# Kernel tuning notes

Hardware: AMD Instinct MI355X
Metric: run time of the kernel (lower is better)

Reference implementation:

```python
import jax, jax.numpy as jnp
import numpy as np

D_MODEL = 1024
NUM_HEADS = 16
D_K = D_MODEL // NUM_HEADS


def setup_inputs() -> dict:
    key = jax.random.key(0)
    ks = jax.random.split(key, 11)
    B, T = 4, 2048
    s = 1.0 / np.sqrt(D_MODEL)
    return {
        'query': jax.random.normal(ks[0], (B, T, D_MODEL), jnp.float32),
        'key': jax.random.normal(ks[1], (B, T, D_MODEL), jnp.float32),
        'value': jax.random.normal(ks[2], (B, T, D_MODEL), jnp.float32),
        'Wq': jax.random.normal(ks[3], (D_MODEL, D_MODEL), jnp.float32) * s,
        'bq': jnp.zeros((D_MODEL,), jnp.float32),
        'Wk': jax.random.normal(ks[4], (D_MODEL, D_MODEL), jnp.float32) * s,
        'bk': jnp.zeros((D_MODEL,), jnp.float32),
        'Wv': jax.random.normal(ks[5], (D_MODEL, D_MODEL), jnp.float32) * s,
        'bv': jnp.zeros((D_MODEL,), jnp.float32),
        'Wo': jax.random.normal(ks[6], (D_MODEL, D_MODEL), jnp.float32) * s,
        'bo': jnp.zeros((D_MODEL,), jnp.float32),
    }


def reference(query, key, value, Wq, bq, Wk, bk, Wv, bv, Wo, bo):
    B, Tq, _ = query.shape
    Tk = key.shape[1]
    # projections (torch Linear: x @ W.T + b)
    q = (query @ Wq.T + bq).reshape(B, Tq, NUM_HEADS, D_K).transpose(0, 2, 1, 3)
    k = (key @ Wk.T + bk).reshape(B, Tk, NUM_HEADS, D_K).transpose(0, 2, 1, 3)
    v = (value @ Wv.T + bv).reshape(B, Tk, NUM_HEADS, D_K).transpose(0, 2, 1, 3)
    scale = 1.0 / jnp.sqrt(jnp.asarray(D_K, q.dtype))
    scores = jnp.einsum('bhqd,bhkd->bhqk', q, k) * scale  # [B,H,Tq,Tk]
    attn = jax.nn.softmax(scores, axis=-1)
    out = jnp.einsum('bhqk,bhkd->bhqd', attn, v)
    out = out.transpose(0, 2, 1, 3).reshape(B, Tq, D_MODEL)
    return out @ Wo.T + bo
```

## Files before the change

### kernel.cpp

```cpp
#include <hip/hip_runtime.h>

typedef unsigned short u16;
typedef unsigned int u32;
typedef __attribute__((ext_vector_type(8))) short bf16x8;
typedef __attribute__((ext_vector_type(4))) float f32x4;

__device__ inline u16 f2bf(float x) {
  union { float f; unsigned u; } v; v.f = x;
  unsigned r = v.u + 0x7fffu + ((v.u >> 16) & 1u);
  return (u16)(r >> 16);
}

__device__ inline u32 packbf2(float p0, float p1) {
  return __builtin_amdgcn_perm(__float_as_uint(p1), __float_as_uint(p0), 0x07060302u);
}

__device__ inline void gload16(const void* g, void* l) {
  __builtin_amdgcn_global_load_lds(
      (const __attribute__((address_space(1))) unsigned int*)g,
      (__attribute__((address_space(3))) unsigned int*)l,
      16, 0, 0);
}

__global__ void cvt_bf16_multi(const float* __restrict__ s0, const float* __restrict__ s1,
                               const float* __restrict__ s2, const float* __restrict__ s3,
                               u16* __restrict__ d0, u16* __restrict__ d1,
                               u16* __restrict__ d2, u16* __restrict__ d3, int n4) {
  int i = blockIdx.x * blockDim.x + threadIdx.x;
  if (i >= n4) return;
  int t = blockIdx.y;
  const float* src = (t == 0) ? s0 : (t == 1) ? s1 : (t == 2) ? s2 : s3;
  u16* dst = (t == 0) ? d0 : (t == 1) ? d1 : (t == 2) ? d2 : d3;
  float4 v = ((const float4*)src)[i];
  ushort4 o;
  o.x = f2bf(v.x); o.y = f2bf(v.y); o.z = f2bf(v.z); o.w = f2bf(v.w);
  ((ushort4*)dst)[i] = o;
}

template<int MODE>
__global__ __launch_bounds__(256, 2) void gemm_bt(
    const u16* __restrict__ A, const u16* __restrict__ W,
    const float* __restrict__ bias, void* __restrict__ Cout)
{
  constexpr int N = 1024, K = 1024, BK = 32, NT = K / BK;
  __shared__ __align__(16) u16 As[2][128 * BK];
  __shared__ __align__(16) u16 Bs[2][128 * BK];
  const int tid = threadIdx.x;
  const int wave = tid >> 6, lane = tid & 63;
  const int quad = lane >> 4, l16 = lane & 15;
  const int m0 = blockIdx.x * 128, n0 = blockIdx.y * 128;

  const int sA = wave * 2;
  const int srow = lane >> 2;
  const int skcol = ((lane & 3) ^ (srow & 3)) * 8;
  const int mloc = sA * 16 + srow;
  const int arow = (MODE == 1) ? ((mloc & 64) + (mloc & 3) * 16 + ((mloc & 63) >> 2)) : mloc;
  const int astep = (MODE == 1) ? 4 : 16;
  const u16* ag = A + (size_t)(m0 + arow) * K + skcol;
  const u16* bg = W + (size_t)(n0 + mloc) * K + skcol;

  const int wm = (wave >> 1) * 64, wn = (wave & 1) * 64;
  f32x4 acc[4][4] = {};

  gload16(ag, As[0] + sA * 512);
  gload16(ag + (size_t)astep * K, As[0] + sA * 512 + 512);
  gload16(bg, Bs[0] + sA * 512);
  gload16(bg + 16 * K, Bs[0] + sA * 512 + 512);
  ag += BK; bg += BK;
  __syncthreads();

  int cur = 0;
  for (int kt = 0; kt < NT; ++kt) {
    if (kt + 1 < NT) {
      const int nb = cur ^ 1;
      gload16(ag, As[nb] + sA * 512);
      gload16(ag + (size_t)astep * K, As[nb] + sA * 512 + 512);
      gload16(bg, Bs[nb] + sA * 512);
      gload16(bg + 16 * K, Bs[nb] + sA * 512 + 512);
      ag += BK; bg += BK;
    }
    const u16* Ac = As[cur];
    const u16* Bc = Bs[cur];
    bf16x8 af[4], bf[4];
#pragma unroll
    for (int mi = 0; mi < 4; ++mi)
      af[mi] = *(const bf16x8*)(Ac + (wm + mi * 16 + l16) * BK + ((quad ^ (l16 & 3)) * 8));
#pragma unroll
    for (int ni = 0; ni < 4; ++ni)
      bf[ni] = *(const bf16x8*)(Bc + (wn + ni * 16 + l16) * BK + ((quad ^ (l16 & 3)) * 8));
#pragma unroll
    for (int mi = 0; mi < 4; ++mi)
#pragma unroll
      for (int ni = 0; ni < 4; ++ni)
        acc[mi][ni] = __builtin_amdgcn_mfma_f32_16x16x32_bf16(af[mi], bf[ni], acc[mi][ni], 0, 0, 0);
    __syncthreads();
    cur ^= 1;
  }

#pragma unroll
  for (int ni = 0; ni < 4; ++ni) {
    const int col = n0 + wn + ni * 16 + l16;
    const float bv = bias[col];
#pragma unroll
    for (int mi = 0; mi < 4; ++mi) {
      const int mrow = m0 + wm + mi * 16 + quad * 4;
      f32x4 a = acc[mi][ni];
      if (MODE == 2) {
        float* C = (float*)Cout;
#pragma unroll
        for (int r = 0; r < 4; ++r)
          C[(size_t)(mrow + r) * N + col] = a[r] + bv;
      } else if (MODE == 0) {
        u16* C = (u16*)Cout;
#pragma unroll
        for (int r = 0; r < 4; ++r)
          C[(size_t)(mrow + r) * N + col] = f2bf(a[r] + bv);
      } else {
        u16* C = (u16*)Cout;
        const int bq = mrow >> 11, t = mrow & 2047;
        const int h = col >> 6, d = col & 63;
        ushort4 pk;
        pk.x = f2bf(a[0] + bv); pk.y = f2bf(a[1] + bv);
        pk.z = f2bf(a[2] + bv); pk.w = f2bf(a[3] + bv);
        *(ushort4*)(C + ((size_t)((bq * 16 + h) * 64 + d)) * 2048 + t) = pk;
      }
    }
  }
}

__global__ __launch_bounds__(512, 4) void flash_attn(
    const u16* __restrict__ Qp, const u16* __restrict__ Kp,
    const u16* __restrict__ Vt, u16* __restrict__ Ctx)
{
  constexpr int TQ = 2048, DM = 1024, DK = 64;
  constexpr int KP = 72;
  constexpr int VP = 136;
  constexpr int PP = 68;
  __shared__ __align__(16) u16 Ks[128 * KP];
  __shared__ __align__(16) u16 Vts[64 * VP];
  __shared__ __align__(16) u16 Ps[8][16 * PP];

  const int bh = blockIdx.x, b = bh >> 4, h = bh & 15;
  const int qt = blockIdx.y;
  const int tid = threadIdx.x, wave = tid >> 6, lane = tid & 63;
  const int quad = lane >> 4, l16 = lane & 15;
  const int q0 = qt * 256 + wave * 32;

  bf16x8 qf[2][2];
#pragma unroll
  for (int mi = 0; mi < 2; ++mi)
#pragma unroll
    for (int ks = 0; ks < 2; ++ks)
      qf[mi][ks] = *(const bf16x8*)(Qp + (size_t)(b * TQ + q0 + mi * 16 + l16) * DM
                                       + h * DK + ks * 32 + quad * 8);

  f32x4 O[2][4] = {};
  f32x4 lsum[2] = {};
  const float CS = 0.18033688011112042f;
  const float C0 = 0.0028153f;

  bf16x8 onesv;
#pragma unroll
  for (int j = 0; j < 8; ++j) onesv[j] = (short)0x3F80;

  for (int kt = 0; kt < TQ / 128; ++kt) {
    const int k0 = kt * 128;
#pragma unroll
    for (int i = 0; i < 2; ++i) {
      int c = tid + i * 512;
      int row = c >> 3, seg = c & 7;
      *(float4*)(Ks + row * KP + seg * 8) =
          *(const float4*)(Kp + (size_t)(b * TQ + k0 + row) * DM + h * DK + seg * 8);
    }
#pragma unroll
    for (int i = 0; i < 2; ++i) {
      int c = tid + i * 512;
      int d = c >> 4, seg = c & 15;
      *(float4*)(Vts + d * VP + seg * 8) =
          *(const float4*)(Vt + ((size_t)(bh * DK + d)) * TQ + k0 + seg * 8);
    }
    __syncthreads();

#pragma unroll
    for (int g = 0; g < 2; ++g) {
      f32x4 Sg[2][4];
#pragma unroll
      for (int cc = 0; cc < 4; ++cc) {
        const int c = g * 4 + cc;
        bf16x8 kf0 = *(const bf16x8*)(Ks + (c * 16 + l16) * KP + quad * 8);
        bf16x8 kf1 = *(const bf16x8*)(Ks + (c * 16 + l16) * KP + 32 + quad * 8);
#pragma unroll
        for (int mi = 0; mi < 2; ++mi) {
          f32x4 z = {};
          z = __builtin_amdgcn_mfma_f32_16x16x32_bf16(qf[mi][0], kf0, z, 0, 0, 0);
          Sg[mi][cc] = __builtin_amdgcn_mfma_f32_16x16x32_bf16(qf[mi][1], kf1, z, 0, 0, 0);
        }
      }
      bf16x8 pf[2][2];
#pragma unroll
      for (int mi = 0; mi < 2; ++mi) {
#pragma unroll
        for (int r = 0; r < 4; ++r) {
          float e0 = __builtin_amdgcn_exp2f(fmaf(Sg[mi][0][r], CS, C0));
          float e1 = __builtin_amdgcn_exp2f(fmaf(Sg[mi][1][r], CS, C0));
          float e2 = __builtin_amdgcn_exp2f(fmaf(Sg[mi][2][r], CS, C0));
          float e3 = __builtin_amdgcn_exp2f(fmaf(Sg[mi][3][r], CS, C0));
          uint2 pk;
          pk.x = packbf2(e0, e1);
          pk.y = packbf2(e2, e3);
          *(uint2*)(&Ps[wave][(quad * 4 + r) * PP + l16 * 4]) = pk;
        }
#pragma unroll
        for (int ksl = 0; ksl < 2; ++ksl)
          pf[mi][ksl] = *(const bf16x8*)(&Ps[wave][l16 * PP + ksl * 32 + quad * 8]);
#pragma unroll
        for (int ksl = 0; ksl < 2; ++ksl)
          lsum[mi] = __builtin_amdgcn_mfma_f32_16x16x32_bf16(pf[mi][ksl], onesv, lsum[mi], 0, 0, 0);
      }
#pragma unroll
      for (int ksl = 0; ksl < 2; ++ksl)
#pragma unroll
        for (int ni = 0; ni < 4; ++ni) {
          bf16x8 vf = *(const bf16x8*)(Vts + (ni * 16 + l16) * VP
                                           + g * 64 + ksl * 32 + quad * 8);
          O[0][ni] = __builtin_amdgcn_mfma_f32_16x16x32_bf16(pf[0][ksl], vf, O[0][ni], 0, 0, 0);
          O[1][ni] = __builtin_amdgcn_mfma_f32_16x16x32_bf16(pf[1][ksl], vf, O[1][ni], 0, 0, 0);
        }
    }
    __syncthreads();
  }

#pragma unroll
  for (int mi = 0; mi < 2; ++mi)
#pragma unroll
    for (int r = 0; r < 4; ++r) {
      const float inv = 1.0f / lsum[mi][r];
      const int q = q0 + mi * 16 + quad * 4 + r;
#pragma unroll
      for (int ni = 0; ni < 4; ++ni) {
        const int col = h * DK + ni * 16 + l16;
        Ctx[(size_t)(b * TQ + q) * DM + col] = f2bf(O[mi][ni][r] * inv);
      }
    }
}

extern "C" void kernel_launch(void* const* d_in, const int* in_sizes, int n_in,
                              void* d_out, int out_size, void* d_ws, size_t ws_size,
                              hipStream_t stream)
{
  (void)in_sizes; (void)n_in; (void)out_size; (void)ws_size;
  const float* query = (const float*)d_in[0];
  const float* key_  = (const float*)d_in[1];
  const float* value = (const float*)d_in[2];
  const float* Wq = (const float*)d_in[3];
  const float* bq = (const float*)d_in[4];
  const float* Wk = (const float*)d_in[5];
  const float* bk = (const float*)d_in[6];
  const float* Wv = (const float*)d_in[7];
  const float* bv = (const float*)d_in[8];
  const float* Wo = (const float*)d_in[9];
  const float* bo = (const float*)d_in[10];

  const size_t MT = (size_t)4 * 2048 * 1024;
  const size_t WT = (size_t)1024 * 1024;
  u16* ws  = (u16*)d_ws;
  u16* Xq  = ws;
  u16* Xk  = Xq + MT;
  u16* Xv  = Xk + MT;
  u16* Wqb = Xv + MT;
  u16* Wkb = Wqb + WT;
  u16* Wvb = Wkb + WT;
  u16* Wob = Wvb + WT;
  u16* Qp  = Wob + WT;
  u16* Kp  = Qp + MT;
  u16* Vt  = Kp + MT;
  u16* Ctx = Vt + MT;

  cvt_bf16_multi<<<dim3(8192, 3), 256, 0, stream>>>(
      query, key_, value, value, Xq, Xk, Xv, Xv, (int)(MT / 4));
  cvt_bf16_multi<<<dim3(1024, 4), 256, 0, stream>>>(
      Wq, Wk, Wv, Wo, Wqb, Wkb, Wvb, Wob, (int)(WT / 4));

  dim3 gg(64, 8);
  gemm_bt<0><<<gg, 256, 0, stream>>>(Xq, Wqb, bq, Qp);
  gemm_bt<0><<<gg, 256, 0, stream>>>(Xk, Wkb, bk, Kp);
  gemm_bt<1><<<gg, 256, 0, stream>>>(Xv, Wvb, bv, Vt);

  flash_attn<<<dim3(64, 8), 512, 0, stream>>>(Qp, Kp, Vt, Ctx);

  gemm_bt<2><<<gg, 256, 0, stream>>>(Ctx, Wob, bo, (float*)d_out);
}
```

Baseline: 351.1 us.

## Batch QKV GEMMs, merge conversions, double-buffer flash attention K/V loads

The two conversion kernels are merged into one launch, and the three QKV projection GEMMs become a single launch over a z-dimension grid with occupancy hint 3. The flash attention kernel now double-buffers its K/V tiles using async global-to-LDS loads, with XOR swizzling in place of padding, and raises wave priority around the MFMA sections. The goal is fewer launches, more waves resident at once, and memory latency hidden behind compute. The cost is more shared memory in attention and more complex swizzled indexing.

```diff
diff --git a/kernel.cpp b/kernel.cpp
--- a/kernel.cpp
+++ b/kernel.cpp
@@ -22,19 +22,121 @@
       16, 0, 0);
 }
 
-__global__ void cvt_bf16_multi(const float* __restrict__ s0, const float* __restrict__ s1,
-                               const float* __restrict__ s2, const float* __restrict__ s3,
-                               u16* __restrict__ d0, u16* __restrict__ d1,
-                               u16* __restrict__ d2, u16* __restrict__ d3, int n4) {
-  int i = blockIdx.x * blockDim.x + threadIdx.x;
-  if (i >= n4) return;
-  int t = blockIdx.y;
-  const float* src = (t == 0) ? s0 : (t == 1) ? s1 : (t == 2) ? s2 : s3;
-  u16* dst = (t == 0) ? d0 : (t == 1) ? d1 : (t == 2) ? d2 : d3;
-  float4 v = ((const float4*)src)[i];
+__global__ void cvt_all(const float* __restrict__ q, const float* __restrict__ k,
+                        const float* __restrict__ v,
+                        const float* __restrict__ wq, const float* __restrict__ wk,
+                        const float* __restrict__ wv, const float* __restrict__ wo,
+                        u16* __restrict__ ws) {
+  const size_t MT4 = (size_t)2 * 1024 * 1024;
+  const int i = blockIdx.x * blockDim.x + threadIdx.x;
+  const int t = blockIdx.y;
+  float4 vv;
   ushort4 o;
-  o.x = f2bf(v.x); o.y = f2bf(v.y); o.z = f2bf(v.z); o.w = f2bf(v.w);
-  ((ushort4*)dst)[i] = o;
+  if (t < 3) {
+    const float* src = (t == 0) ? q : (t == 1) ? k : v;
+    vv = ((const float4*)src)[i];
+    o.x = f2bf(vv.x); o.y = f2bf(vv.y); o.z = f2bf(vv.z); o.w = f2bf(vv.w);
+    ((ushort4*)ws)[(size_t)t * MT4 + i] = o;
+  } else {
+    if (i >= (1 << 20)) return;
+    const int w = i >> 18, j = i & 0x3FFFF;
+    const float* src = (w == 0) ? wq : (w == 1) ? wk : (w == 2) ? wv : wo;
+    vv = ((const float4*)src)[j];
+    o.x = f2bf(vv.x); o.y = f2bf(vv.y); o.z = f2bf(vv.z); o.w = f2bf(vv.w);
+    ((ushort4*)(ws + 3 * MT4 * 4))[i] = o;
+  }
+}
+
+__global__ __launch_bounds__(256, 3) void gemm_qkv(
+    const u16* __restrict__ Xq, const u16* __restrict__ Wqb,
+    const float* __restrict__ bq_, const float* __restrict__ bk_,
+    const float* __restrict__ bv_, u16* __restrict__ Qp)
+{
+  constexpr int N = 1024, K = 1024, BK = 32, NT = K / BK;
+  constexpr size_t MT = (size_t)8192 * 1024, WT = (size_t)1024 * 1024;
+  __shared__ __align__(16) u16 As[2][128 * BK];
+  __shared__ __align__(16) u16 Bs[2][128 * BK];
+  const int z = blockIdx.z;
+  const u16* A = Xq + (size_t)z * MT;
+  const u16* W = Wqb + (size_t)z * WT;
+  const float* bias = (z == 0) ? bq_ : (z == 1) ? bk_ : bv_;
+  u16* Cout = Qp + (size_t)z * MT;
+  const bool vm = (z == 2);
+
+  const int tid = threadIdx.x;
+  const int wave = tid >> 6, lane = tid & 63;
+  const int quad = lane >> 4, l16 = lane & 15;
+  const int m0 = blockIdx.x * 128, n0 = blockIdx.y * 128;
+
+  const int sA = wave * 2;
+  const int srow = lane >> 2;
+  const int skcol = ((lane & 3) ^ (srow & 3)) * 8;
+  const int mloc = sA * 16 + srow;
+  const int arow = vm ? ((mloc & 64) + (mloc & 3) * 16 + ((mloc & 63) >> 2)) : mloc;
+  const int astep = vm ? 4 : 16;
+  const u16* ag = A + (size_t)(m0 + arow) * K + skcol;
+  const u16* bg = W + (size_t)(n0 + mloc) * K + skcol;
+
+  const int wm = (wave >> 1) * 64, wn = (wave & 1) * 64;
+  f32x4 acc[4][4] = {};
+
+  gload16(ag, As[0] + sA * 512);
+  gload16(ag + (size_t)astep * K, As[0] + sA * 512 + 512);
+  gload16(bg, Bs[0] + sA * 512);
+  gload16(bg + 16 * K, Bs[0] + sA * 512 + 512);
+  ag += BK; bg += BK;
+  __syncthreads();
+
+  int cur = 0;
+  for (int kt = 0; kt < NT; ++kt) {
+    if (kt + 1 < NT) {
+      const int nb = cur ^ 1;
+      gload16(ag, As[nb] + sA * 512);
+      gload16(ag + (size_t)astep * K, As[nb] + sA * 512 + 512);
+      gload16(bg, Bs[nb] + sA * 512);
+      gload16(bg + 16 * K, Bs[nb] + sA * 512 + 512);
+      ag += BK; bg += BK;
+    }
+    const u16* Ac = As[cur];
+    const u16* Bc = Bs[cur];
+    bf16x8 af[4], bf[4];
+#pragma unroll
+    for (int mi = 0; mi < 4; ++mi)
+      af[mi] = *(const bf16x8*)(Ac + (wm + mi * 16 + l16) * BK + ((quad ^ (l16 & 3)) * 8));
+#pragma unroll
+    for (int ni = 0; ni < 4; ++ni)
+      bf[ni] = *(const bf16x8*)(Bc + (wn + ni * 16 + l16) * BK + ((quad ^ (l16 & 3)) * 8));
+#pragma unroll
+    for (int mi = 0; mi < 4; ++mi)
+#pragma unroll
+      for (int ni = 0; ni < 4; ++ni)
+        acc[mi][ni] = __builtin_amdgcn_mfma_f32_16x16x32_bf16(af[mi], bf[ni], acc[mi][ni], 0, 0, 0);
+    __syncthreads();
+    cur ^= 1;
+  }
+
+#pragma unroll
+  for (int ni = 0; ni < 4; ++ni) {
+    const int col = n0 + wn + ni * 16 + l16;
+    const float bv = bias[col];
+#pragma unroll
+    for (int mi = 0; mi < 4; ++mi) {
+      const int mrow = m0 + wm + mi * 16 + quad * 4;
+      f32x4 a = acc[mi][ni];
+      if (!vm) {
+#pragma unroll
+        for (int r = 0; r < 4; ++r)
+          Cout[(size_t)(mrow + r) * N + col] = f2bf(a[r] + bv);
+      } else {
+        const int bq = mrow >> 11, t = mrow & 2047;
+        const int h = col >> 6, d = col & 63;
+        ushort4 pk;
+        pk.x = f2bf(a[0] + bv); pk.y = f2bf(a[1] + bv);
+        pk.z = f2bf(a[2] + bv); pk.w = f2bf(a[3] + bv);
+        *(ushort4*)(Cout + ((size_t)((bq * 16 + h) * 64 + d)) * 2048 + t) = pk;
+      }
+    }
+  }
 }
 
 template<int MODE>
@@ -54,16 +156,14 @@
   const int srow = lane >> 2;
   const int skcol = ((lane & 3) ^ (srow & 3)) * 8;
   const int mloc = sA * 16 + srow;
-  const int arow = (MODE == 1) ? ((mloc & 64) + (mloc & 3) * 16 + ((mloc & 63) >> 2)) : mloc;
-  const int astep = (MODE == 1) ? 4 : 16;
-  const u16* ag = A + (size_t)(m0 + arow) * K + skcol;
+  const u16* ag = A + (size_t)(m0 + mloc) * K + skcol;
   const u16* bg = W + (size_t)(n0 + mloc) * K + skcol;
 
   const int wm = (wave >> 1) * 64, wn = (wave & 1) * 64;
   f32x4 acc[4][4] = {};
 
   gload16(ag, As[0] + sA * 512);
-  gload16(ag + (size_t)astep * K, As[0] + sA * 512 + 512);
+  gload16(ag + 16 * K, As[0] + sA * 512 + 512);
   gload16(bg, Bs[0] + sA * 512);
   gload16(bg + 16 * K, Bs[0] + sA * 512 + 512);
   ag += BK; bg += BK;
@@ -74,7 +174,7 @@
     if (kt + 1 < NT) {
       const int nb = cur ^ 1;
       gload16(ag, As[nb] + sA * 512);
-      gload16(ag + (size_t)astep * K, As[nb] + sA * 512 + 512);
+      gload16(ag + 16 * K, As[nb] + sA * 512 + 512);
       gload16(bg, Bs[nb] + sA * 512);
       gload16(bg + 16 * K, Bs[nb] + sA * 512 + 512);
       ag += BK; bg += BK;
@@ -105,25 +205,10 @@
     for (int mi = 0; mi < 4; ++mi) {
       const int mrow = m0 + wm + mi * 16 + quad * 4;
       f32x4 a = acc[mi][ni];
-      if (MODE == 2) {
-        float* C = (float*)Cout;
-#pragma unroll
-        for (int r = 0; r < 4; ++r)
-          C[(size_t)(mrow + r) * N + col] = a[r] + bv;
-      } else if (MODE == 0) {
-        u16* C = (u16*)Cout;
-#pragma unroll
-        for (int r = 0; r < 4; ++r)
-          C[(size_t)(mrow + r) * N + col] = f2bf(a[r] + bv);
-      } else {
-        u16* C = (u16*)Cout;
-        const int bq = mrow >> 11, t = mrow & 2047;
-        const int h = col >> 6, d = col & 63;
-        ushort4 pk;
-        pk.x = f2bf(a[0] + bv); pk.y = f2bf(a[1] + bv);
-        pk.z = f2bf(a[2] + bv); pk.w = f2bf(a[3] + bv);
-        *(ushort4*)(C + ((size_t)((bq * 16 + h) * 64 + d)) * 2048 + t) = pk;
-      }
+      float* C = (float*)Cout;
+#pragma unroll
+      for (int r = 0; r < 4; ++r)
+        C[(size_t)(mrow + r) * N + col] = a[r] + bv;
     }
   }
 }
@@ -133,12 +218,9 @@
     const u16* __restrict__ Vt, u16* __restrict__ Ctx)
 {
   constexpr int TQ = 2048, DM = 1024, DK = 64;
-  constexpr int KP = 72;
-  constexpr int VP = 136;
-  constexpr int PP = 68;
-  __shared__ __align__(16) u16 Ks[128 * KP];
-  __shared__ __align__(16) u16 Vts[64 * VP];
-  __shared__ __align__(16) u16 Ps[8][16 * PP];
+  __shared__ __align__(16) u16 Ks[2][128 * 64];
+  __shared__ __align__(16) u16 Vts[2][64 * 128];
+  __shared__ __align__(16) u16 Ps[8][16 * 64];
 
   const int bh = blockIdx.x, b = bh >> 4, h = bh & 15;
   const int qt = blockIdx.y;
@@ -146,6 +228,14 @@
   const int quad = lane >> 4, l16 = lane & 15;
   const int q0 = qt * 256 + wave * 32;
 
+  const int C0 = tid, C1 = 512 + tid;
+  const int kr0 = C0 >> 3, kr1 = C1 >> 3;
+  const u16* kp0 = Kp + (size_t)(b * TQ + kr0) * DM + h * DK + (((C0 & 7) ^ (kr0 & 7)) * 8);
+  const u16* kp1 = Kp + (size_t)(b * TQ + kr1) * DM + h * DK + (((C1 & 7) ^ (kr1 & 7)) * 8);
+  const int vd0 = C0 >> 4, vd1 = C1 >> 4;
+  const u16* vp0 = Vt + (size_t)(bh * DK + vd0) * TQ + (((C0 & 15) ^ (vd0 & 15)) * 8);
+  const u16* vp1 = Vt + (size_t)(bh * DK + vd1) * TQ + (((C1 & 15) ^ (vd1 & 15)) * 8);
+
   bf16x8 qf[2][2];
 #pragma unroll
   for (int mi = 0; mi < 2; ++mi)
@@ -157,77 +247,87 @@
   f32x4 O[2][4] = {};
   f32x4 lsum[2] = {};
   const float CS = 0.18033688011112042f;
-  const float C0 = 0.0028153f;
+  const float CB = 0.0028153f;
 
   bf16x8 onesv;
 #pragma unroll
   for (int j = 0; j < 8; ++j) onesv[j] = (short)0x3F80;
 
+  gload16(kp0, &Ks[0][C0 * 8]);
+  gload16(kp1, &Ks[0][C1 * 8]);
+  gload16(vp0, &Vts[0][C0 * 8]);
+  gload16(vp1, &Vts[0][C1 * 8]);
+  kp0 += 128 * DM; kp1 += 128 * DM; vp0 += 128; vp1 += 128;
+  __syncthreads();
+
+  const int kg = quad ^ (l16 & 7);
+  int cur = 0;
   for (int kt = 0; kt < TQ / 128; ++kt) {
-    const int k0 = kt * 128;
-#pragma unroll
-    for (int i = 0; i < 2; ++i) {
-      int c = tid + i * 512;
-      int row = c >> 3, seg = c & 7;
-      *(float4*)(Ks + row * KP + seg * 8) =
-          *(const float4*)(Kp + (size_t)(b * TQ + k0 + row) * DM + h * DK + seg * 8);
-    }
-#pragma unroll
-    for (int i = 0; i < 2; ++i) {
-      int c = tid + i * 512;
-      int d = c >> 4, seg = c & 15;
-      *(float4*)(Vts + d * VP + seg * 8) =
-          *(const float4*)(Vt + ((size_t)(bh * DK + d)) * TQ + k0 + seg * 8);
-    }
-    __syncthreads();
+    if (kt + 1 < TQ / 128) {
+      const int nb = cur ^ 1;
+      gload16(kp0, &Ks[nb][C0 * 8]);
+      gload16(kp1, &Ks[nb][C1 * 8]);
+      gload16(vp0, &Vts[nb][C0 * 8]);
+      gload16(vp1, &Vts[nb][C1 * 8]);
+      kp0 += 128 * DM; kp1 += 128 * DM; vp0 += 128; vp1 += 128;
+    }
+    const u16* Kc = Ks[cur];
+    const u16* Vc = Vts[cur];
+    u16* Psw = Ps[wave];
 
 #pragma unroll
     for (int g = 0; g < 2; ++g) {
       f32x4 Sg[2][4];
+      __builtin_amdgcn_s_setprio(1);
 #pragma unroll
       for (int cc = 0; cc < 4; ++cc) {
-        const int c = g * 4 + cc;
-        bf16x8 kf0 = *(const bf16x8*)(Ks + (c * 16 + l16) * KP + quad * 8);
-        bf16x8 kf1 = *(const bf16x8*)(Ks + (c * 16 + l16) * KP + 32 + quad * 8);
+        const int row = (g * 4 + cc) * 16 + l16;
+        bf16x8 kf0 = *(const bf16x8*)(Kc + row * 64 + kg * 8);
+        bf16x8 kf1 = *(const bf16x8*)(Kc + row * 64 + (kg ^ 4) * 8);
 #pragma unroll
         for (int mi = 0; mi < 2; ++mi) {
-          f32x4 z = {};
-          z = __builtin_amdgcn_mfma_f32_16x16x32_bf16(qf[mi][0], kf0, z, 0, 0, 0);
-          Sg[mi][cc] = __builtin_amdgcn_mfma_f32_16x16x32_bf16(qf[mi][1], kf1, z, 0, 0, 0);
+          f32x4 zz = {};
+          zz = __builtin_amdgcn_mfma_f32_16x16x32_bf16(qf[mi][0], kf0, zz, 0, 0, 0);
+          Sg[mi][cc] = __builtin_amdgcn_mfma_f32_16x16x32_bf16(qf[mi][1], kf1, zz, 0, 0, 0);
         }
       }
+      __builtin_amdgcn_s_setprio(0);
       bf16x8 pf[2][2];
 #pragma unroll
       for (int mi = 0; mi < 2; ++mi) {
 #pragma unroll
         for (int r = 0; r < 4; ++r) {
-          float e0 = __builtin_amdgcn_exp2f(fmaf(Sg[mi][0][r], CS, C0));
-          float e1 = __builtin_amdgcn_exp2f(fmaf(Sg[mi][1][r], CS, C0));
-          float e2 = __builtin_amdgcn_exp2f(fmaf(Sg[mi][2][r], CS, C0));
-          float e3 = __builtin_amdgcn_exp2f(fmaf(Sg[mi][3][r], CS, C0));
+          float e0 = __builtin_amdgcn_exp2f(fmaf(Sg[mi][0][r], CS, CB));
+          float e1 = __builtin_amdgcn_exp2f(fmaf(Sg[mi][1][r], CS, CB));
+          float e2 = __builtin_amdgcn_exp2f(fmaf(Sg[mi][2][r], CS, CB));
+          float e3 = __builtin_amdgcn_exp2f(fmaf(Sg[mi][3][r], CS, CB));
           uint2 pk;
           pk.x = packbf2(e0, e1);
           pk.y = packbf2(e2, e3);
-          *(uint2*)(&Ps[wave][(quad * 4 + r) * PP + l16 * 4]) = pk;
+          const int pw = quad * 4 + r;
+          *(uint2*)(&Psw[pw * 64 + ((l16 * 4) ^ ((pw & 7) << 3))]) = pk;
         }
 #pragma unroll
         for (int ksl = 0; ksl < 2; ++ksl)
-          pf[mi][ksl] = *(const bf16x8*)(&Ps[wave][l16 * PP + ksl * 32 + quad * 8]);
+          pf[mi][ksl] = *(const bf16x8*)(&Psw[l16 * 64 + ((ksl * 32 + quad * 8) ^ ((l16 & 7) << 3))]);
 #pragma unroll
         for (int ksl = 0; ksl < 2; ++ksl)
           lsum[mi] = __builtin_amdgcn_mfma_f32_16x16x32_bf16(pf[mi][ksl], onesv, lsum[mi], 0, 0, 0);
       }
+      __builtin_amdgcn_s_setprio(1);
 #pragma unroll
       for (int ksl = 0; ksl < 2; ++ksl)
 #pragma unroll
         for (int ni = 0; ni < 4; ++ni) {
-          bf16x8 vf = *(const bf16x8*)(Vts + (ni * 16 + l16) * VP
-                                           + g * 64 + ksl * 32 + quad * 8);
+          const int gv = g * 8 + ksl * 4 + quad;
+          bf16x8 vf = *(const bf16x8*)(Vc + (ni * 16 + l16) * 128 + ((gv ^ l16) * 8));
           O[0][ni] = __builtin_amdgcn_mfma_f32_16x16x32_bf16(pf[0][ksl], vf, O[0][ni], 0, 0, 0);
           O[1][ni] = __builtin_amdgcn_mfma_f32_16x16x32_bf16(pf[1][ksl], vf, O[1][ni], 0, 0, 0);
         }
+      __builtin_amdgcn_s_setprio(0);
     }
     __syncthreads();
+    cur ^= 1;
   }
 
 #pragma unroll
@@ -265,28 +365,19 @@
   const size_t WT = (size_t)1024 * 1024;
   u16* ws  = (u16*)d_ws;
   u16* Xq  = ws;
-  u16* Xk  = Xq + MT;
-  u16* Xv  = Xk + MT;
-  u16* Wqb = Xv + MT;
-  u16* Wkb = Wqb + WT;
-  u16* Wvb = Wkb + WT;
-  u16* Wob = Wvb + WT;
-  u16* Qp  = Wob + WT;
+  u16* Wqb = Xq + 3 * MT;
+  u16* Qp  = Wqb + 4 * WT;
   u16* Kp  = Qp + MT;
   u16* Vt  = Kp + MT;
   u16* Ctx = Vt + MT;
-
-  cvt_bf16_multi<<<dim3(8192, 3), 256, 0, stream>>>(
-      query, key_, value, value, Xq, Xk, Xv, Xv, (int)(MT / 4));
-  cvt_bf16_multi<<<dim3(1024, 4), 256, 0, stream>>>(
-      Wq, Wk, Wv, Wo, Wqb, Wkb, Wvb, Wob, (int)(WT / 4));
-
-  dim3 gg(64, 8);
-  gemm_bt<0><<<gg, 256, 0, stream>>>(Xq, Wqb, bq, Qp);
-  gemm_bt<0><<<gg, 256, 0, stream>>>(Xk, Wkb, bk, Kp);
-  gemm_bt<1><<<gg, 256, 0, stream>>>(Xv, Wvb, bv, Vt);
+  u16* Wob = Wqb + 3 * WT;
+
+  cvt_all<<<dim3(8192, 4), 256, 0, stream>>>(
+      query, key_, value, Wq, Wk, Wv, Wo, ws);
+
+  gemm_qkv<<<dim3(64, 8, 3), 256, 0, stream>>>(Xq, Wqb, bq, bk, bv, Qp);
 
   flash_attn<<<dim3(64, 8), 512, 0, stream>>>(Qp, Kp, Vt, Ctx);
 
-  gemm_bt<2><<<gg, 256, 0, stream>>>(Ctx, Wob, bo, (float*)d_out);
-}
+  gemm_bt<2><<<dim3(64, 8), 256, 0, stream>>>(Ctx, Wob, bo, (float*)d_out);
+}
```

After: 341.3 us. 2.8% less time.
